# Kernel optimization log

Hardware: AMD Instinct MI355X
Metric: run time of the kernel (lower is better)

## Reference

```python
import jax, jax.numpy as jnp
import numpy as np

N_SRC = 8192
N_DST = 8192
E = 524288
D = 128
M = 64


def layer_norm(x, g, b, eps=1e-5):
    mu = x.mean(-1, keepdims=True)
    var = ((x - mu) ** 2).mean(-1, keepdims=True)
    return (x - mu) * jax.lax.rsqrt(var + eps) * g + b


def setup_inputs() -> dict:
    key = jax.random.key(0)
    ks = jax.random.split(key, 32)

    def p(k, shape, s=0.02):
        return jax.random.normal(k, shape, jnp.float32) * s

    inp = {
        "src_embed": jax.random.normal(ks[0], (N_SRC, D), jnp.float32),
        "dst_embed": jax.random.normal(ks[1], (N_DST, D), jnp.float32),
        "v_s2d": jax.random.normal(ks[2], (E, M), jnp.float32),
        "v_d2s": jax.random.normal(ks[3], (E, M), jnp.float32),
        "e_s2d_dst": jax.random.randint(ks[4], (E,), 0, N_DST, jnp.int32),
        "e_d2s_dst": jax.random.randint(ks[5], (E,), 0, N_SRC, jnp.int32),
        # node transforms
        "W_src": p(ks[6], (D, D)), "b_src": jnp.zeros((D,), jnp.float32),
        "W_dst": p(ks[7], (D, D)), "b_dst": jnp.zeros((D,), jnp.float32),
        # edge-message transforms
        "W_sm": p(ks[8], (M, D)), "b_sm": jnp.zeros((D,), jnp.float32),
        "W_dm": p(ks[9], (M, D)), "b_dm": jnp.zeros((D,), jnp.float32),
        # apply_row: LNLayer (Linear+LayerNorm) then Linear
        "row_W1": p(ks[10], (D, D)), "row_b1": jnp.zeros((D,), jnp.float32),
        "row_g": jnp.ones((D,), jnp.float32), "row_beta": jnp.zeros((D,), jnp.float32),
        "row_W2": p(ks[11], (D, D)), "row_b2": jnp.zeros((D,), jnp.float32),
        # apply_col
        "col_W1": p(ks[12], (D, D)), "col_b1": jnp.zeros((D,), jnp.float32),
        "col_g": jnp.ones((D,), jnp.float32), "col_beta": jnp.zeros((D,), jnp.float32),
        "col_W2": p(ks[13], (D, D)), "col_b2": jnp.zeros((D,), jnp.float32),
    }
    return inp


def reference(src_embed, dst_embed, v_s2d, v_d2s, e_s2d_dst, e_d2s_dst,
              W_src, b_src, W_dst, b_dst, W_sm, b_sm, W_dm, b_dm,
              row_W1, row_b1, row_g, row_beta, row_W2, row_b2,
              col_W1, col_b1, col_g, col_beta, col_W2, col_b2):
    # node transforms: h[ntype]
    h_src = src_embed @ W_src + b_src          # [N_src, D]
    h_dst = dst_embed @ W_dst + b_dst          # [N_dst, D]
    # edge message transforms
    msg_s2d = v_s2d @ W_sm + b_sm              # [E, D]
    msg_d2s = v_d2s @ W_dm + b_dm              # [E, D]
    # message = h[dst-of-edge] * msg, scatter-sum onto destination nodes
    out_dst = jax.ops.segment_sum(h_dst[e_s2d_dst] * msg_s2d, e_s2d_dst,
                                  num_segments=N_DST)   # src2dst -> dst nodes
    out_src = jax.ops.segment_sum(h_src[e_d2s_dst] * msg_d2s, e_d2s_dst,
                                  num_segments=N_SRC)   # dst2src -> src nodes
    # residual apply: x + Linear(LayerNorm(Linear(out)))
    row = src_embed + (layer_norm(out_src @ row_W1 + row_b1, row_g, row_beta) @ row_W2 + row_b2)
    col = dst_embed + (layer_norm(out_dst @ col_W1 + col_b1, col_g, col_beta) @ col_W2 + col_b2)
    return row, col
```

## Files before the change

### kernel.cpp

```cpp
#include <hip/hip_runtime.h>


#define DEV __device__ __forceinline__

typedef __bf16 bf16x8 __attribute__((ext_vector_type(8)));
typedef unsigned short u16x8 __attribute__((ext_vector_type(8)));
typedef float f32x4 __attribute__((ext_vector_type(4)));

constexpr int N_NODES = 8192;
constexpr int NUM_E   = 524288;
constexpr int D       = 128;
constexpr int M       = 64;

DEV unsigned short f2bf(float f) {
    unsigned int x = __float_as_uint(f);
    unsigned int r = (x + 0x7fffu + ((x >> 16) & 1u)) >> 16;
    return (unsigned short)r;
}
DEV bf16x8 load8(const unsigned short* p) {
    return *reinterpret_cast<const bf16x8*>(p);
}
DEV bf16x8 cvt8(const float* p) {
    union { u16x8 u; bf16x8 b; } cv;
#pragma unroll
    for (int i = 0; i < 8; ++i) cv.u[i] = f2bf(p[i]);
    return cv.b;
}
DEV f32x4 mfma16(bf16x8 a, bf16x8 b, f32x4 c) {
    return __builtin_amdgcn_mfma_f32_16x16x32_bf16(a, b, c, 0, 0, 0);
}

__global__ __launch_bounds__(256) void hist_k(const int* __restrict__ i0,
                                              const int* __restrict__ i1,
                                              int* __restrict__ counts) {
    int t = blockIdx.x * 256 + threadIdx.x;
    int base = 0;
    const int4* p = (const int4*)i0;
    if (t >= NUM_E / 4) { p = (const int4*)i1; base = N_NODES; t -= NUM_E / 4; }
    int4 e = p[t];
    atomicAdd(counts + base + (e.x & (N_NODES - 1)), 1);
    atomicAdd(counts + base + (e.y & (N_NODES - 1)), 1);
    atomicAdd(counts + base + (e.z & (N_NODES - 1)), 1);
    atomicAdd(counts + base + (e.w & (N_NODES - 1)), 1);
}

__global__ __launch_bounds__(256) void scan_k(const int* __restrict__ counts,
                                              int* __restrict__ offsets,
                                              int* __restrict__ cursors) {
    __shared__ int part[256];
    int t = threadIdx.x;
    for (int dir = 0; dir < 2; ++dir) {
        const int* c = counts + dir * N_NODES;
        int* off = offsets + dir * (N_NODES + 1);
        int* cur = cursors + dir * N_NODES;
        int local[32];
        int s = 0;
#pragma unroll
        for (int i = 0; i < 32; ++i) { int v = c[t * 32 + i]; local[i] = s; s += v; }
        part[t] = s;
        __syncthreads();
        for (int dd = 1; dd < 256; dd <<= 1) {
            int w = (t >= dd) ? part[t - dd] : 0;
            __syncthreads();
            part[t] += w;
            __syncthreads();
        }
        int base = part[t] - s;
#pragma unroll
        for (int i = 0; i < 32; ++i) { int o = base + local[i]; off[t * 32 + i] = o; cur[t * 32 + i] = o; }
        if (t == 255) off[N_NODES] = part[255];
        __syncthreads();
    }
}

__global__ __launch_bounds__(256) void scatter_k(const int* __restrict__ i0,
                                                 const int* __restrict__ i1,
                                                 int* __restrict__ cursors,
                                                 int* __restrict__ csr) {
    int t = blockIdx.x * 256 + threadIdx.x;
    int dir = 0;
    if (t >= NUM_E / 4) { dir = 1; t -= NUM_E / 4; }
    const int4* idx = (const int4*)(dir ? i1 : i0);
    int4 nn = idx[t];
    int* cur = cursors + dir * N_NODES;
    int* c = csr + dir * NUM_E;
    int e = t * 4;
    c[atomicAdd(cur + (nn.x & (N_NODES - 1)), 1)] = e;
    c[atomicAdd(cur + (nn.y & (N_NODES - 1)), 1)] = e + 1;
    c[atomicAdd(cur + (nn.z & (N_NODES - 1)), 1)] = e + 2;
    c[atomicAdd(cur + (nn.w & (N_NODES - 1)), 1)] = e + 3;
}

struct TransArgs {
    const float* src[8];
    unsigned short* dst[8];
    int K[8];
};
__global__ __launch_bounds__(256) void transpose_k(TransArgs ta) {
    int b = blockIdx.x;
    const float* s = ta.src[b];
    unsigned short* d = ta.dst[b];
    int K = ta.K[b];
    int total = K << 7;
    for (int i = threadIdx.x; i < total; i += 256) {
        int k = i >> 7, n = i & 127;
        d[n * K + k] = f2bf(s[i]);
    }
}

__global__ __launch_bounds__(256) void gather_k(const float* __restrict__ v0,
                                                const float* __restrict__ v1,
                                                const int* __restrict__ offsets,
                                                const int* __restrict__ csr,
                                                unsigned short* __restrict__ Abf) {
    int wave = (blockIdx.x * 256 + threadIdx.x) >> 6;
    int lane = threadIdx.x & 63;
    int dir = wave >> 13;
    int n = wave & (N_NODES - 1);
    const float* v = dir ? v1 : v0;
    const int* off = offsets + dir * (N_NODES + 1);
    const int* cs = csr + dir * NUM_E;
    const int f16 = lane & 15;
    const int g = lane >> 4;
    int j0 = off[n], j1 = off[n + 1];
    f32x4 acc = {0.f, 0.f, 0.f, 0.f};

    int nfull = (j1 - j0) >> 4;
    int j = j0;
    if (nfull > 0) {
        int idx0, idx1, idx2, idx3;
        idx0 = cs[j + g];
        idx1 = cs[j + g + 4];
        idx2 = cs[j + g + 8];
        idx3 = cs[j + g + 12];
        for (int it = 0; it < nfull; ++it) {
            int jn = j + 16;
            int p0 = 0, p1 = 0, p2 = 0, p3 = 0;
            bool more = (it + 1) < nfull;
            if (more) {
                p0 = cs[jn + g];
                p1 = cs[jn + g + 4];
                p2 = cs[jn + g + 8];
                p3 = cs[jn + g + 12];
            }
            f32x4 d0 = *(const f32x4*)(v + (size_t)idx0 * M + f16 * 4);
            f32x4 d1 = *(const f32x4*)(v + (size_t)idx1 * M + f16 * 4);
            f32x4 d2 = *(const f32x4*)(v + (size_t)idx2 * M + f16 * 4);
            f32x4 d3 = *(const f32x4*)(v + (size_t)idx3 * M + f16 * 4);
            acc += d0; acc += d1; acc += d2; acc += d3;
            idx0 = p0; idx1 = p1; idx2 = p2; idx3 = p3;
            j = jn;
        }
    }
    for (; j < j1; j += 4) {
        int e = j + g;
        if (e < j1) {
            f32x4 d = *(const f32x4*)(v + (size_t)cs[e] * M + f16 * 4);
            acc += d;
        }
    }
#pragma unroll
    for (int i = 0; i < 4; ++i) {
        acc[i] += __shfl_xor(acc[i], 16, 64);
        acc[i] += __shfl_xor(acc[i], 32, 64);
    }
    if (g == 0) {
        union { unsigned short u[4]; unsigned long long ll; } w;
#pragma unroll
        for (int i = 0; i < 4; ++i) w.u[i] = f2bf(acc[i]);
        *reinterpret_cast<unsigned long long*>(Abf + (size_t)wave * M + f16 * 4) = w.ll;
    }
}

struct SideArgs {
    const float* X;
    const unsigned short* Wnode_t;
    const float* bnode;
    const unsigned short* Abf;
    const int* counts;
    const unsigned short* Wmsg_t;
    const float* bmsg;
    const unsigned short* W1_t;
    const float* b1;
    const float* g;
    const float* beta;
    const unsigned short* W2_t;
    const float* b2;
    float* out;
};

__global__ __launch_bounds__(256) void apply_k(SideArgs A0, SideArgs A1) {
    const int side = blockIdx.x >> 7;
    const SideArgs& a = side ? A1 : A0;
    const int blk = blockIdx.x & 127;
    const int wv = threadIdx.x >> 6;
    const int lane = threadIdx.x & 63;
    const int nb = blk * 64 + wv * 16;
    const int m = lane & 15;
    const int quad = lane >> 4;

    __shared__ __align__(16) unsigned short sAbuf[4][16 * 136];
    unsigned short* sA = sAbuf[wv];

    f32x4 acc_h[8];
#pragma unroll
    for (int dt = 0; dt < 8; ++dt) acc_h[dt] = (f32x4){0.f, 0.f, 0.f, 0.f};
    {
        bf16x8 af[4];
#pragma unroll
        for (int ks = 0; ks < 4; ++ks)
            af[ks] = cvt8(a.X + (size_t)(nb + m) * D + ks * 32 + quad * 8);
#pragma unroll
        for (int dt = 0; dt < 8; ++dt) {
#pragma unroll
            for (int ks = 0; ks < 4; ++ks) {
                bf16x8 bfr = load8(a.Wnode_t + (size_t)(dt * 16 + m) * D + ks * 32 + quad * 8);
                acc_h[dt] = mfma16(af[ks], bfr, acc_h[dt]);
            }
        }
    }
    f32x4 acc_t[8];
#pragma unroll
    for (int dt = 0; dt < 8; ++dt) acc_t[dt] = (f32x4){0.f, 0.f, 0.f, 0.f};
    {
        bf16x8 at[2];
#pragma unroll
        for (int ks = 0; ks < 2; ++ks)
            at[ks] = load8(a.Abf + (size_t)(nb + m) * M + ks * 32 + quad * 8);
#pragma unroll
        for (int dt = 0; dt < 8; ++dt) {
#pragma unroll
            for (int ks = 0; ks < 2; ++ks) {
                bf16x8 bfr = load8(a.Wmsg_t + (size_t)(dt * 16 + m) * M + ks * 32 + quad * 8);
                acc_t[dt] = mfma16(at[ks], bfr, acc_t[dt]);
            }
        }
    }
    {
        float bnode_f[8], bmsg_f[8];
#pragma unroll
        for (int dt = 0; dt < 8; ++dt) {
            bnode_f[dt] = a.bnode[dt * 16 + m];
            bmsg_f[dt] = a.bmsg[dt * 16 + m];
        }
        float cnt_f[4];
#pragma unroll
        for (int r = 0; r < 4; ++r) cnt_f[r] = (float)a.counts[nb + quad * 4 + r];
#pragma unroll
        for (int dt = 0; dt < 8; ++dt) {
#pragma unroll
            for (int r = 0; r < 4; ++r) {
                float hv = acc_h[dt][r] + bnode_f[dt];
                float tv = acc_t[dt][r] + cnt_f[r] * bmsg_f[dt];
                sA[(quad * 4 + r) * 136 + dt * 16 + m] = f2bf(hv * tv);
            }
        }
    }
    __syncthreads();
    f32x4 acc_u[8];
#pragma unroll
    for (int dt = 0; dt < 8; ++dt) acc_u[dt] = (f32x4){0.f, 0.f, 0.f, 0.f};
    {
        bf16x8 au[4];
#pragma unroll
        for (int ks = 0; ks < 4; ++ks)
            au[ks] = load8(sA + m * 136 + ks * 32 + quad * 8);
#pragma unroll
        for (int dt = 0; dt < 8; ++dt) {
#pragma unroll
            for (int ks = 0; ks < 4; ++ks) {
                bf16x8 bfr = load8(a.W1_t + (size_t)(dt * 16 + m) * D + ks * 32 + quad * 8);
                acc_u[dt] = mfma16(au[ks], bfr, acc_u[dt]);
            }
        }
    }
    float g_f[8], beta_f[8];
    {
#pragma unroll
        for (int dt = 0; dt < 8; ++dt) {
            float b1v = a.b1[dt * 16 + m];
            g_f[dt] = a.g[dt * 16 + m];
            beta_f[dt] = a.beta[dt * 16 + m];
#pragma unroll
            for (int r = 0; r < 4; ++r) acc_u[dt][r] += b1v;
        }
    }
    float s[4], sq[4];
#pragma unroll
    for (int r = 0; r < 4; ++r) { s[r] = 0.f; sq[r] = 0.f; }
#pragma unroll
    for (int dt = 0; dt < 8; ++dt)
#pragma unroll
        for (int r = 0; r < 4; ++r) { float u = acc_u[dt][r]; s[r] += u; sq[r] += u * u; }
#pragma unroll
    for (int off = 1; off < 16; off <<= 1) {
#pragma unroll
        for (int r = 0; r < 4; ++r) {
            s[r] += __shfl_xor(s[r], off, 64);
            sq[r] += __shfl_xor(sq[r], off, 64);
        }
    }
    float mu[4], rstd[4];
#pragma unroll
    for (int r = 0; r < 4; ++r) {
        mu[r] = s[r] * (1.0f / 128.0f);
        float var = sq[r] * (1.0f / 128.0f) - mu[r] * mu[r];
        rstd[r] = rsqrtf(fmaxf(var, 0.f) + 1e-5f);
    }
    __syncthreads();
#pragma unroll
    for (int dt = 0; dt < 8; ++dt)
#pragma unroll
        for (int r = 0; r < 4; ++r) {
            float ln = (acc_u[dt][r] - mu[r]) * rstd[r] * g_f[dt] + beta_f[dt];
            sA[(quad * 4 + r) * 136 + dt * 16 + m] = f2bf(ln);
        }
    __syncthreads();
    f32x4 acc_y[8];
#pragma unroll
    for (int dt = 0; dt < 8; ++dt) acc_y[dt] = (f32x4){0.f, 0.f, 0.f, 0.f};
    {
        bf16x8 ay[4];
#pragma unroll
        for (int ks = 0; ks < 4; ++ks)
            ay[ks] = load8(sA + m * 136 + ks * 32 + quad * 8);
#pragma unroll
        for (int dt = 0; dt < 8; ++dt) {
#pragma unroll
            for (int ks = 0; ks < 4; ++ks) {
                bf16x8 bfr = load8(a.W2_t + (size_t)(dt * 16 + m) * D + ks * 32 + quad * 8);
                acc_y[dt] = mfma16(ay[ks], bfr, acc_y[dt]);
            }
        }
    }
#pragma unroll
    for (int dt = 0; dt < 8; ++dt) {
        float b2v = a.b2[dt * 16 + m];
#pragma unroll
        for (int r = 0; r < 4; ++r) {
            int node = nb + quad * 4 + r;
            int d = dt * 16 + m;
            float xv = a.X[(size_t)node * D + d];
            a.out[(size_t)node * D + d] = acc_y[dt][r] + b2v + xv;
        }
    }
}

extern "C" void kernel_launch(void* const* d_in, const int* in_sizes, int n_in,
                              void* d_out, int out_size, void* d_ws, size_t ws_size,
                              hipStream_t stream) {
    const float* src_embed = (const float*)d_in[0];
    const float* dst_embed = (const float*)d_in[1];
    const float* v_s2d = (const float*)d_in[2];
    const float* v_d2s = (const float*)d_in[3];
    const int* e_s2d = (const int*)d_in[4];
    const int* e_d2s = (const int*)d_in[5];
    const float* W_src = (const float*)d_in[6];
    const float* b_src = (const float*)d_in[7];
    const float* W_dst = (const float*)d_in[8];
    const float* b_dst = (const float*)d_in[9];
    const float* W_sm = (const float*)d_in[10];
    const float* b_sm = (const float*)d_in[11];
    const float* W_dm = (const float*)d_in[12];
    const float* b_dm = (const float*)d_in[13];
    const float* row_W1 = (const float*)d_in[14];
    const float* row_b1 = (const float*)d_in[15];
    const float* row_g = (const float*)d_in[16];
    const float* row_beta = (const float*)d_in[17];
    const float* row_W2 = (const float*)d_in[18];
    const float* row_b2 = (const float*)d_in[19];
    const float* col_W1 = (const float*)d_in[20];
    const float* col_b1 = (const float*)d_in[21];
    const float* col_g = (const float*)d_in[22];
    const float* col_beta = (const float*)d_in[23];
    const float* col_W2 = (const float*)d_in[24];
    const float* col_b2 = (const float*)d_in[25];
    float* out = (float*)d_out;

    char* ws = (char*)d_ws;
    int* counts = (int*)(ws + 0);
    int* offsets = (int*)(ws + 65536);
    int* cursors = (int*)(ws + 131328);
    unsigned short* Wt = (unsigned short*)(ws + 197120);
    unsigned short* Abf = (unsigned short*)(ws + 426752);
    int* csr = (int*)(out + (size_t)N_NODES * D);

    hipMemsetAsync(counts, 0, 2 * N_NODES * sizeof(int), stream);
    hist_k<<<(2 * NUM_E / 4) / 256, 256, 0, stream>>>(e_s2d, e_d2s, counts);
    scan_k<<<1, 256, 0, stream>>>(counts, offsets, cursors);
    scatter_k<<<(2 * NUM_E / 4) / 256, 256, 0, stream>>>(e_s2d, e_d2s, cursors, csr);

    TransArgs ta;
    const float* srcs[8] = {W_src, W_dst, W_sm, W_dm, row_W1, row_W2, col_W1, col_W2};
    int Ks[8] = {128, 128, 64, 64, 128, 128, 128, 128};
    int offs[8] = {0, 16384, 32768, 40960, 49152, 65536, 81920, 98304};
    for (int i = 0; i < 8; ++i) { ta.src[i] = srcs[i]; ta.dst[i] = Wt + offs[i]; ta.K[i] = Ks[i]; }
    transpose_k<<<8, 256, 0, stream>>>(ta);

    gather_k<<<(2 * N_NODES * 64) / 256, 256, 0, stream>>>(v_s2d, v_d2s, offsets, csr, Abf);

    SideArgs rowA = {src_embed, Wt + 0, b_src, Abf + (size_t)N_NODES * M, counts + N_NODES,
                     Wt + 40960, b_dm, Wt + 49152, row_b1, row_g, row_beta, Wt + 65536, row_b2,
                     out};
    SideArgs colA = {dst_embed, Wt + 16384, b_dst, Abf, counts,
                     Wt + 32768, b_sm, Wt + 81920, col_b1, col_g, col_beta, Wt + 98304, col_b2,
                     out + (size_t)N_NODES * D};
    apply_k<<<256, 256, 0, stream>>>(rowA, colA);
}
```

Measured before the change: 500.3 us.

## Split apply work across waves per 16-node group and parallelize scan by direction

The apply kernel now assigns one 16-node group per block, with each of the four waves computing two of the eight output column tiles. LayerNorm statistics are reduced across waves through shared memory. This raises the grid from 256 to 1024 blocks and cuts per-thread accumulator registers, which should improve occupancy and latency hiding on a small-grid kernel. The scan runs as two blocks, one per direction, and gather is split into two launches with the transpose moved earlier. The cost is extra block syncs and four times more reloads of weight fragments across blocks.

After: 496.1 us. No clear change (-0.8%).

```diff
diff --git a/kernel.cpp b/kernel.cpp
--- a/kernel.cpp
+++ b/kernel.cpp
@@ -49,28 +49,26 @@
                                               int* __restrict__ cursors) {
     __shared__ int part[256];
     int t = threadIdx.x;
-    for (int dir = 0; dir < 2; ++dir) {
-        const int* c = counts + dir * N_NODES;
-        int* off = offsets + dir * (N_NODES + 1);
-        int* cur = cursors + dir * N_NODES;
-        int local[32];
-        int s = 0;
-#pragma unroll
-        for (int i = 0; i < 32; ++i) { int v = c[t * 32 + i]; local[i] = s; s += v; }
-        part[t] = s;
+    int dir = blockIdx.x;
+    const int* c = counts + dir * N_NODES;
+    int* off = offsets + dir * (N_NODES + 1);
+    int* cur = cursors + dir * N_NODES;
+    int local[32];
+    int s = 0;
+#pragma unroll
+    for (int i = 0; i < 32; ++i) { int v = c[t * 32 + i]; local[i] = s; s += v; }
+    part[t] = s;
+    __syncthreads();
+    for (int dd = 1; dd < 256; dd <<= 1) {
+        int w = (t >= dd) ? part[t - dd] : 0;
         __syncthreads();
-        for (int dd = 1; dd < 256; dd <<= 1) {
-            int w = (t >= dd) ? part[t - dd] : 0;
-            __syncthreads();
-            part[t] += w;
-            __syncthreads();
-        }
-        int base = part[t] - s;
-#pragma unroll
-        for (int i = 0; i < 32; ++i) { int o = base + local[i]; off[t * 32 + i] = o; cur[t * 32 + i] = o; }
-        if (t == 255) off[N_NODES] = part[255];
+        part[t] += w;
         __syncthreads();
     }
+    int base = part[t] - s;
+#pragma unroll
+    for (int i = 0; i < 32; ++i) { int o = base + local[i]; off[t * 32 + i] = o; cur[t * 32 + i] = o; }
+    if (t == 255) off[N_NODES] = part[255];
 }
 
 __global__ __launch_bounds__(256) void scatter_k(const int* __restrict__ i0,
@@ -108,18 +106,12 @@
     }
 }
 
-__global__ __launch_bounds__(256) void gather_k(const float* __restrict__ v0,
-                                                const float* __restrict__ v1,
-                                                const int* __restrict__ offsets,
-                                                const int* __restrict__ csr,
-                                                unsigned short* __restrict__ Abf) {
-    int wave = (blockIdx.x * 256 + threadIdx.x) >> 6;
+__global__ __launch_bounds__(256) void gather_k(const float* __restrict__ v,
+                                                const int* __restrict__ off,
+                                                const int* __restrict__ cs,
+                                                unsigned short* __restrict__ Ab) {
+    int n = (blockIdx.x * 256 + threadIdx.x) >> 6;
     int lane = threadIdx.x & 63;
-    int dir = wave >> 13;
-    int n = wave & (N_NODES - 1);
-    const float* v = dir ? v1 : v0;
-    const int* off = offsets + dir * (N_NODES + 1);
-    const int* cs = csr + dir * NUM_E;
     const int f16 = lane & 15;
     const int g = lane >> 4;
     int j0 = off[n], j1 = off[n + 1];
@@ -128,16 +120,12 @@
     int nfull = (j1 - j0) >> 4;
     int j = j0;
     if (nfull > 0) {
-        int idx0, idx1, idx2, idx3;
-        idx0 = cs[j + g];
-        idx1 = cs[j + g + 4];
-        idx2 = cs[j + g + 8];
-        idx3 = cs[j + g + 12];
+        int idx0 = cs[j + g], idx1 = cs[j + g + 4];
+        int idx2 = cs[j + g + 8], idx3 = cs[j + g + 12];
         for (int it = 0; it < nfull; ++it) {
             int jn = j + 16;
             int p0 = 0, p1 = 0, p2 = 0, p3 = 0;
-            bool more = (it + 1) < nfull;
-            if (more) {
+            if ((it + 1) < nfull) {
                 p0 = cs[jn + g];
                 p1 = cs[jn + g + 4];
                 p2 = cs[jn + g + 8];
@@ -154,10 +142,7 @@
     }
     for (; j < j1; j += 4) {
         int e = j + g;
-        if (e < j1) {
-            f32x4 d = *(const f32x4*)(v + (size_t)cs[e] * M + f16 * 4);
-            acc += d;
-        }
+        if (e < j1) acc += *(const f32x4*)(v + (size_t)cs[e] * M + f16 * 4);
     }
 #pragma unroll
     for (int i = 0; i < 4; ++i) {
@@ -168,7 +153,7 @@
         union { unsigned short u[4]; unsigned long long ll; } w;
 #pragma unroll
         for (int i = 0; i < 4; ++i) w.u[i] = f2bf(acc[i]);
-        *reinterpret_cast<unsigned long long*>(Abf + (size_t)wave * M + f16 * 4) = w.ll;
+        *reinterpret_cast<unsigned long long*>(Ab + (size_t)n * M + f16 * 4) = w.ll;
     }
 }
 
@@ -190,108 +175,95 @@
 };
 
 __global__ __launch_bounds__(256) void apply_k(SideArgs A0, SideArgs A1) {
-    const int side = blockIdx.x >> 7;
+    const int side = blockIdx.x >> 9;
     const SideArgs& a = side ? A1 : A0;
-    const int blk = blockIdx.x & 127;
-    const int wv = threadIdx.x >> 6;
+    const int grp = blockIdx.x & 511;
+    const int nb = grp * 16;
+    const int w = threadIdx.x >> 6;
     const int lane = threadIdx.x & 63;
-    const int nb = blk * 64 + wv * 16;
     const int m = lane & 15;
     const int quad = lane >> 4;
 
-    __shared__ __align__(16) unsigned short sAbuf[4][16 * 136];
-    unsigned short* sA = sAbuf[wv];
-
-    f32x4 acc_h[8];
-#pragma unroll
-    for (int dt = 0; dt < 8; ++dt) acc_h[dt] = (f32x4){0.f, 0.f, 0.f, 0.f};
+    __shared__ __align__(16) unsigned short sP[16 * 136];
+    __shared__ float part_s[4][16], part_sq[4][16];
+
+    bf16x8 af[4];
+#pragma unroll
+    for (int ks = 0; ks < 4; ++ks)
+        af[ks] = cvt8(a.X + (size_t)(nb + m) * D + ks * 32 + quad * 8);
+    f32x4 acc_h[2] = {{0.f, 0.f, 0.f, 0.f}, {0.f, 0.f, 0.f, 0.f}};
+#pragma unroll
+    for (int i = 0; i < 2; ++i) {
+        int dt = 2 * w + i;
+#pragma unroll
+        for (int ks = 0; ks < 4; ++ks) {
+            bf16x8 bfr = load8(a.Wnode_t + (size_t)(dt * 16 + m) * D + ks * 32 + quad * 8);
+            acc_h[i] = mfma16(af[ks], bfr, acc_h[i]);
+        }
+    }
+    bf16x8 at[2];
+#pragma unroll
+    for (int ks = 0; ks < 2; ++ks)
+        at[ks] = load8(a.Abf + (size_t)(nb + m) * M + ks * 32 + quad * 8);
+    f32x4 acc_t[2] = {{0.f, 0.f, 0.f, 0.f}, {0.f, 0.f, 0.f, 0.f}};
+#pragma unroll
+    for (int i = 0; i < 2; ++i) {
+        int dt = 2 * w + i;
+#pragma unroll
+        for (int ks = 0; ks < 2; ++ks) {
+            bf16x8 bfr = load8(a.Wmsg_t + (size_t)(dt * 16 + m) * M + ks * 32 + quad * 8);
+            acc_t[i] = mfma16(at[ks], bfr, acc_t[i]);
+        }
+    }
     {
-        bf16x8 af[4];
-#pragma unroll
-        for (int ks = 0; ks < 4; ++ks)
-            af[ks] = cvt8(a.X + (size_t)(nb + m) * D + ks * 32 + quad * 8);
-#pragma unroll
-        for (int dt = 0; dt < 8; ++dt) {
-#pragma unroll
-            for (int ks = 0; ks < 4; ++ks) {
-                bf16x8 bfr = load8(a.Wnode_t + (size_t)(dt * 16 + m) * D + ks * 32 + quad * 8);
-                acc_h[dt] = mfma16(af[ks], bfr, acc_h[dt]);
+        float cnt_f[4];
+#pragma unroll
+        for (int r = 0; r < 4; ++r) cnt_f[r] = (float)a.counts[nb + quad * 4 + r];
+#pragma unroll
+        for (int i = 0; i < 2; ++i) {
+            int dt = 2 * w + i;
+            float bn = a.bnode[dt * 16 + m];
+            float bm = a.bmsg[dt * 16 + m];
+#pragma unroll
+            for (int r = 0; r < 4; ++r) {
+                float hv = acc_h[i][r] + bn;
+                float tv = acc_t[i][r] + cnt_f[r] * bm;
+                sP[(quad * 4 + r) * 136 + dt * 16 + m] = f2bf(hv * tv);
             }
         }
     }
-    f32x4 acc_t[8];
-#pragma unroll
-    for (int dt = 0; dt < 8; ++dt) acc_t[dt] = (f32x4){0.f, 0.f, 0.f, 0.f};
-    {
-        bf16x8 at[2];
-#pragma unroll
-        for (int ks = 0; ks < 2; ++ks)
-            at[ks] = load8(a.Abf + (size_t)(nb + m) * M + ks * 32 + quad * 8);
-#pragma unroll
-        for (int dt = 0; dt < 8; ++dt) {
-#pragma unroll
-            for (int ks = 0; ks < 2; ++ks) {
-                bf16x8 bfr = load8(a.Wmsg_t + (size_t)(dt * 16 + m) * M + ks * 32 + quad * 8);
-                acc_t[dt] = mfma16(at[ks], bfr, acc_t[dt]);
-            }
-        }
-    }
-    {
-        float bnode_f[8], bmsg_f[8];
-#pragma unroll
-        for (int dt = 0; dt < 8; ++dt) {
-            bnode_f[dt] = a.bnode[dt * 16 + m];
-            bmsg_f[dt] = a.bmsg[dt * 16 + m];
-        }
-        float cnt_f[4];
-#pragma unroll
-        for (int r = 0; r < 4; ++r) cnt_f[r] = (float)a.counts[nb + quad * 4 + r];
-#pragma unroll
-        for (int dt = 0; dt < 8; ++dt) {
-#pragma unroll
-            for (int r = 0; r < 4; ++r) {
-                float hv = acc_h[dt][r] + bnode_f[dt];
-                float tv = acc_t[dt][r] + cnt_f[r] * bmsg_f[dt];
-                sA[(quad * 4 + r) * 136 + dt * 16 + m] = f2bf(hv * tv);
-            }
-        }
-    }
     __syncthreads();
-    f32x4 acc_u[8];
-#pragma unroll
-    for (int dt = 0; dt < 8; ++dt) acc_u[dt] = (f32x4){0.f, 0.f, 0.f, 0.f};
-    {
-        bf16x8 au[4];
-#pragma unroll
-        for (int ks = 0; ks < 4; ++ks)
-            au[ks] = load8(sA + m * 136 + ks * 32 + quad * 8);
-#pragma unroll
-        for (int dt = 0; dt < 8; ++dt) {
-#pragma unroll
-            for (int ks = 0; ks < 4; ++ks) {
-                bf16x8 bfr = load8(a.W1_t + (size_t)(dt * 16 + m) * D + ks * 32 + quad * 8);
-                acc_u[dt] = mfma16(au[ks], bfr, acc_u[dt]);
-            }
-        }
-    }
-    float g_f[8], beta_f[8];
-    {
-#pragma unroll
-        for (int dt = 0; dt < 8; ++dt) {
-            float b1v = a.b1[dt * 16 + m];
-            g_f[dt] = a.g[dt * 16 + m];
-            beta_f[dt] = a.beta[dt * 16 + m];
-#pragma unroll
-            for (int r = 0; r < 4; ++r) acc_u[dt][r] += b1v;
-        }
+    bf16x8 au[4];
+#pragma unroll
+    for (int ks = 0; ks < 4; ++ks)
+        au[ks] = load8(sP + m * 136 + ks * 32 + quad * 8);
+    f32x4 acc_u[2] = {{0.f, 0.f, 0.f, 0.f}, {0.f, 0.f, 0.f, 0.f}};
+#pragma unroll
+    for (int i = 0; i < 2; ++i) {
+        int dt = 2 * w + i;
+#pragma unroll
+        for (int ks = 0; ks < 4; ++ks) {
+            bf16x8 bfr = load8(a.W1_t + (size_t)(dt * 16 + m) * D + ks * 32 + quad * 8);
+            acc_u[i] = mfma16(au[ks], bfr, acc_u[i]);
+        }
+    }
+    float g_f[2], beta_f[2];
+#pragma unroll
+    for (int i = 0; i < 2; ++i) {
+        int dt = 2 * w + i;
+        float b1v = a.b1[dt * 16 + m];
+        g_f[i] = a.g[dt * 16 + m];
+        beta_f[i] = a.beta[dt * 16 + m];
+#pragma unroll
+        for (int r = 0; r < 4; ++r) acc_u[i][r] += b1v;
     }
     float s[4], sq[4];
 #pragma unroll
     for (int r = 0; r < 4; ++r) { s[r] = 0.f; sq[r] = 0.f; }
 #pragma unroll
-    for (int dt = 0; dt < 8; ++dt)
-#pragma unroll
-        for (int r = 0; r < 4; ++r) { float u = acc_u[dt][r]; s[r] += u; sq[r] += u * u; }
+    for (int i = 0; i < 2; ++i)
+#pragma unroll
+        for (int r = 0; r < 4; ++r) { float u = acc_u[i][r]; s[r] += u; sq[r] += u * u; }
 #pragma unroll
     for (int off = 1; off < 16; off <<= 1) {
 #pragma unroll
@@ -300,48 +272,58 @@
             sq[r] += __shfl_xor(sq[r], off, 64);
         }
     }
+    if (m == 0) {
+#pragma unroll
+        for (int r = 0; r < 4; ++r) {
+            part_s[w][quad * 4 + r] = s[r];
+            part_sq[w][quad * 4 + r] = sq[r];
+        }
+    }
+    __syncthreads();
     float mu[4], rstd[4];
 #pragma unroll
     for (int r = 0; r < 4; ++r) {
-        mu[r] = s[r] * (1.0f / 128.0f);
-        float var = sq[r] * (1.0f / 128.0f) - mu[r] * mu[r];
+        int node = quad * 4 + r;
+        float S = part_s[0][node] + part_s[1][node] + part_s[2][node] + part_s[3][node];
+        float SQ = part_sq[0][node] + part_sq[1][node] + part_sq[2][node] + part_sq[3][node];
+        mu[r] = S * (1.0f / 128.0f);
+        float var = SQ * (1.0f / 128.0f) - mu[r] * mu[r];
         rstd[r] = rsqrtf(fmaxf(var, 0.f) + 1e-5f);
     }
+#pragma unroll
+    for (int i = 0; i < 2; ++i) {
+        int dt = 2 * w + i;
+#pragma unroll
+        for (int r = 0; r < 4; ++r) {
+            float ln = (acc_u[i][r] - mu[r]) * rstd[r] * g_f[i] + beta_f[i];
+            sP[(quad * 4 + r) * 136 + dt * 16 + m] = f2bf(ln);
+        }
+    }
     __syncthreads();
-#pragma unroll
-    for (int dt = 0; dt < 8; ++dt)
-#pragma unroll
-        for (int r = 0; r < 4; ++r) {
-            float ln = (acc_u[dt][r] - mu[r]) * rstd[r] * g_f[dt] + beta_f[dt];
-            sA[(quad * 4 + r) * 136 + dt * 16 + m] = f2bf(ln);
-        }
-    __syncthreads();
-    f32x4 acc_y[8];
-#pragma unroll
-    for (int dt = 0; dt < 8; ++dt) acc_y[dt] = (f32x4){0.f, 0.f, 0.f, 0.f};
-    {
-        bf16x8 ay[4];
-#pragma unroll
-        for (int ks = 0; ks < 4; ++ks)
-            ay[ks] = load8(sA + m * 136 + ks * 32 + quad * 8);
-#pragma unroll
-        for (int dt = 0; dt < 8; ++dt) {
-#pragma unroll
-            for (int ks = 0; ks < 4; ++ks) {
-                bf16x8 bfr = load8(a.W2_t + (size_t)(dt * 16 + m) * D + ks * 32 + quad * 8);
-                acc_y[dt] = mfma16(ay[ks], bfr, acc_y[dt]);
-            }
-        }
-    }
-#pragma unroll
-    for (int dt = 0; dt < 8; ++dt) {
+    bf16x8 ay[4];
+#pragma unroll
+    for (int ks = 0; ks < 4; ++ks)
+        ay[ks] = load8(sP + m * 136 + ks * 32 + quad * 8);
+    f32x4 acc_y[2] = {{0.f, 0.f, 0.f, 0.f}, {0.f, 0.f, 0.f, 0.f}};
+#pragma unroll
+    for (int i = 0; i < 2; ++i) {
+        int dt = 2 * w + i;
+#pragma unroll
+        for (int ks = 0; ks < 4; ++ks) {
+            bf16x8 bfr = load8(a.W2_t + (size_t)(dt * 16 + m) * D + ks * 32 + quad * 8);
+            acc_y[i] = mfma16(ay[ks], bfr, acc_y[i]);
+        }
+    }
+#pragma unroll
+    for (int i = 0; i < 2; ++i) {
+        int dt = 2 * w + i;
         float b2v = a.b2[dt * 16 + m];
 #pragma unroll
         for (int r = 0; r < 4; ++r) {
             int node = nb + quad * 4 + r;
             int d = dt * 16 + m;
             float xv = a.X[(size_t)node * D + d];
-            a.out[(size_t)node * D + d] = acc_y[dt][r] + b2v + xv;
+            a.out[(size_t)node * D + d] = acc_y[i][r] + b2v + xv;
         }
     }
 }
@@ -385,11 +367,6 @@
     unsigned short* Abf = (unsigned short*)(ws + 426752);
     int* csr = (int*)(out + (size_t)N_NODES * D);
 
-    hipMemsetAsync(counts, 0, 2 * N_NODES * sizeof(int), stream);
-    hist_k<<<(2 * NUM_E / 4) / 256, 256, 0, stream>>>(e_s2d, e_d2s, counts);
-    scan_k<<<1, 256, 0, stream>>>(counts, offsets, cursors);
-    scatter_k<<<(2 * NUM_E / 4) / 256, 256, 0, stream>>>(e_s2d, e_d2s, cursors, csr);
-
     TransArgs ta;
     const float* srcs[8] = {W_src, W_dst, W_sm, W_dm, row_W1, row_W2, col_W1, col_W2};
     int Ks[8] = {128, 128, 64, 64, 128, 128, 128, 128};
@@ -397,7 +374,15 @@
     for (int i = 0; i < 8; ++i) { ta.src[i] = srcs[i]; ta.dst[i] = Wt + offs[i]; ta.K[i] = Ks[i]; }
     transpose_k<<<8, 256, 0, stream>>>(ta);
 
-    gather_k<<<(2 * N_NODES * 64) / 256, 256, 0, stream>>>(v_s2d, v_d2s, offsets, csr, Abf);
+    hipMemsetAsync(counts, 0, 2 * N_NODES * sizeof(int), stream);
+    hist_k<<<(2 * NUM_E / 4) / 256, 256, 0, stream>>>(e_s2d, e_d2s, counts);
+    scan_k<<<2, 256, 0, stream>>>(counts, offsets, cursors);
+    scatter_k<<<(2 * NUM_E / 4) / 256, 256, 0, stream>>>(e_s2d, e_d2s, cursors, csr);
+
+    gather_k<<<(N_NODES * 64) / 256, 256, 0, stream>>>(
+        v_s2d, offsets, csr, Abf);
+    gather_k<<<(N_NODES * 64) / 256, 256, 0, stream>>>(
+        v_d2s, offsets + (N_NODES + 1), csr + NUM_E, Abf + (size_t)N_NODES * M);
 
     SideArgs rowA = {src_embed, Wt + 0, b_src, Abf + (size_t)N_NODES * M, counts + N_NODES,
                      Wt + 40960, b_dm, Wt + 49152, row_b1, row_g, row_beta, Wt + 65536, row_b2,
@@ -405,5 +390,5 @@
     SideArgs colA = {dst_embed, Wt + 16384, b_dst, Abf, counts,
                      Wt + 32768, b_sm, Wt + 81920, col_b1, col_g, col_beta, Wt + 98304, col_b2,
                      out + (size_t)N_NODES * D};
-    apply_k<<<256, 256, 0, stream>>>(rowA, colA);
-}
+    apply_k<<<1024, 256, 0, stream>>>(rowA, colA);
+}
```
